# Optimization experiments

Hardware: AMD Instinct MI355X
Metric: run time of the kernel (lower is better)

Reference implementation:

```python
import jax, jax.numpy as jnp
import numpy as np

N_TYPES = 7
DT = 0.1
TAU_INIT = 20.0


def setup_inputs() -> dict:
    key = jax.random.key(0)
    k0, k1, k2, k3 = jax.random.split(key, 4)
    N = 49000          # n_neurons, divisible by 7 types
    E = 1_600_000      # n_edges (~avg degree 32)
    B = 8              # batch (via explicit v_init)
    n_tm1 = N // N_TYPES
    type_ids = (jnp.arange(N) % N_TYPES).astype(jnp.int32)   # type 0 == 'Tm1'
    tm1_indices = jnp.arange(0, N, N_TYPES, dtype=jnp.int32)  # positions where type_ids==0
    return {
        "tm1_input": jax.random.normal(k0, (B, n_tm1), jnp.float32),
        "v_init": jnp.zeros((B, N), jnp.float32),
        "weights": jax.random.normal(k1, (E,), jnp.float32),
        "bias": jnp.zeros((N,), jnp.float32),
        "tau_params": jnp.full((N_TYPES,), TAU_INIT, jnp.float32),
        "scale_excitatory": jnp.ones((), jnp.float32),
        "scale_inhibitory": jnp.ones((), jnp.float32),
        "source_indices": jax.random.randint(k2, (E,), 0, N, dtype=jnp.int32),
        "target_indices": jax.random.randint(k3, (E,), 0, N, dtype=jnp.int32),
        "type_ids": type_ids,
        "tm1_indices": tm1_indices,
        "steps": 100,
    }


def reference(tm1_input, v_init, weights, bias, tau_params,
              scale_excitatory, scale_inhibitory,
              source_indices, target_indices, type_ids, tm1_indices, steps):
    # per-neuron tau from per-type params (torch: get_tau_vector via masks)
    tau = tau_params[type_ids]                                   # [N]
    one = jnp.ones((), weights.dtype)
    edge_scales = jnp.where(weights > 0, scale_excitatory,
                            jnp.where(weights < 0, scale_inhibitory, one))
    scaled_weights = weights * edge_scales                       # [E]

    def step(v, _):
        v = v.at[:, tm1_indices].set(tm1_input)                  # clamp Tm1 neurons
        r = jax.nn.relu(v)                                       # activation
        edge_currents = r[:, source_indices] * scaled_weights    # gather [B,E]
        syn = jnp.zeros_like(v).at[:, target_indices].add(edge_currents)  # scatter-add [B,N]
        dv = (-v + syn + bias) / tau
        dv = dv.at[:, tm1_indices].set(0.0)                      # Tm1 held fixed
        return v + DT * dv, None

    v, _ = jax.lax.scan(step, v_init, None, length=steps)
    return v
```

## Files before the change

kernel.cpp:

```cpp
#include <hip/hip_runtime.h>


#define BLK 256
#define STEPS 100
#define NBATCH 8
#define PRE2 2
static constexpr float DT_C = 0.1f;

__device__ __forceinline__ unsigned f2bf_rne(float x) {
    unsigned u = __float_as_uint(x);
    return (u + 0x7FFFu + ((u >> 16) & 1u)) >> 16;
}
__device__ __forceinline__ unsigned pk_bf2(float a, float b) {
    return f2bf_rne(a) | (f2bf_rne(b) << 16);
}

__global__ void k_zero(int* counts, int* countS, int* tm1_pos, int N) {
    int i = blockIdx.x * BLK + threadIdx.x;
    if (i < N) { counts[i] = 0; countS[i] = 0; tm1_pos[i] = -1; }
}

__global__ void k_tm1pos(const int* __restrict__ tm1_idx, int* tm1_pos, int NT) {
    int i = blockIdx.x * BLK + threadIdx.x;
    if (i < NT) tm1_pos[tm1_idx[i]] = i;
}

__global__ void k_hist(const int* __restrict__ srcI, const int* __restrict__ tgt,
                       const int* __restrict__ type_ids,
                       int* counts, int* countS, unsigned char* __restrict__ flagA,
                       int E) {
    int i = blockIdx.x * BLK + threadIdx.x;
    if (i >= E) return;
    int t = tgt[i];
    atomicAdd(&counts[t], 1);
    unsigned char st = (type_ids[srcI[i]] == 0) ? 1 : 0;
    if (st) atomicAdd(&countS[t], 1);
    flagA[i] = st;
}

__global__ void k_scan1(const int* __restrict__ counts, int* offsets, int* bsum, int N) {
    __shared__ int s[BLK];
    int tx = threadIdx.x;
    int i = blockIdx.x * BLK + tx;
    int v = (i < N) ? counts[i] : 0;
    s[tx] = v; __syncthreads();
    for (int d = 1; d < BLK; d <<= 1) {
        int t = (tx >= d) ? s[tx - d] : 0;
        __syncthreads();
        s[tx] += t;
        __syncthreads();
    }
    if (i < N) offsets[i] = s[tx] - v;
    if (tx == BLK - 1) bsum[blockIdx.x] = s[tx];
}

__global__ void k_scan2(int* bsum, int nb) {
    __shared__ int s[BLK];
    int tx = threadIdx.x;
    int v = (tx < nb) ? bsum[tx] : 0;
    s[tx] = v; __syncthreads();
    for (int d = 1; d < BLK; d <<= 1) {
        int t = (tx >= d) ? s[tx - d] : 0;
        __syncthreads();
        s[tx] += t;
        __syncthreads();
    }
    if (tx < nb) bsum[tx] = s[tx] - v;
}

__global__ void k_scan3(const int* __restrict__ bsum, int* offsets, int N, int E) {
    int i = blockIdx.x * BLK + threadIdx.x;
    if (i < N) {
        offsets[i] += bsum[i >> 8];
    } else if (i == N) {
        offsets[N] = E;
    }
}

__global__ void k_cursors(const int* __restrict__ offsets, const int* __restrict__ countS,
                          int* cursorD, int* cursorS, int* dynEnd, int N) {
    int i = blockIdx.x * BLK + threadIdx.x;
    if (i >= N) return;
    int o  = offsets[i];
    int dE = offsets[i + 1] - countS[i];
    cursorD[i] = o;
    cursorS[i] = dE;
    dynEnd[i]  = dE;
}

__global__ void k_fill(const int* __restrict__ srcI, const int* __restrict__ tgtI,
                       const float* __restrict__ w,
                       const float* __restrict__ se, const float* __restrict__ si,
                       const unsigned char* __restrict__ flagA,
                       int* cursorD, int* cursorS, unsigned* __restrict__ csr, int E) {
    int i = blockIdx.x * BLK + threadIdx.x;
    if (i >= E) return;
    float wv = w[i];
    float sc = wv > 0.f ? se[0] : (wv < 0.f ? si[0] : 1.f);
    float sw = wv * sc;
    unsigned entry = (f2bf_rne(sw) << 16) | (unsigned)srcI[i];
    int t = tgtI[i];
    int pos = flagA[i] ? atomicAdd(&cursorS[t], 1) : atomicAdd(&cursorD[t], 1);
    csr[pos] = entry;
}

__global__ void k_initv(const float* __restrict__ tm1_in, const float* __restrict__ v_init,
                        const float* __restrict__ tau_p,
                        const int* __restrict__ type_ids, const int* __restrict__ tm1_pos,
                        float* __restrict__ v_w, uint4* __restrict__ r0, uint4* __restrict__ r1,
                        float4* __restrict__ coef, int N, int NT) {
    int n = blockIdx.x * BLK + threadIdx.x;
    if (n >= N) return;
    int k = tm1_pos[n];
    float g = DT_C / tau_p[type_ids[n]];
    coef[n] = make_float4(1.f - g, g, (k >= 0) ? 1.f : 0.f, 0.f);
    float vv[NBATCH], rr[NBATCH];
    for (int b = 0; b < NBATCH; ++b) {
        float val = (k >= 0) ? tm1_in[b * NT + k] : v_init[b * N + n];
        vv[b] = val;
        rr[b] = fmaxf(val, 0.f);
    }
    float4* vp = (float4*)(v_w + (size_t)n * 8);
    vp[0] = make_float4(vv[0], vv[1], vv[2], vv[3]);
    vp[1] = make_float4(vv[4], vv[5], vv[6], vv[7]);
    uint4 rq = make_uint4(pk_bf2(rr[0], rr[1]), pk_bf2(rr[2], rr[3]),
                          pk_bf2(rr[4], rr[5]), pk_bf2(rr[6], rr[7]));
    r0[n] = rq;
    r1[n] = rq;
}

__device__ __forceinline__ float butterfly8(float4 a0, float4 a1, int sub) {
    int bit0 = sub & 1, bit1 = (sub >> 1) & 1, bit2 = (sub >> 2) & 1;
    float b0 = (bit0 ? a0.y : a0.x) + __shfl_xor(bit0 ? a0.x : a0.y, 1);
    float b1 = (bit0 ? a0.w : a0.z) + __shfl_xor(bit0 ? a0.z : a0.w, 1);
    float b2 = (bit0 ? a1.y : a1.x) + __shfl_xor(bit0 ? a1.x : a1.y, 1);
    float b3 = (bit0 ? a1.w : a1.z) + __shfl_xor(bit0 ? a1.z : a1.w, 1);
    float c0 = (bit1 ? b1 : b0) + __shfl_xor(bit1 ? b0 : b1, 2);
    float c1 = (bit1 ? b3 : b2) + __shfl_xor(bit1 ? b2 : b3, 2);
    return (bit2 ? c1 : c0) + __shfl_xor(bit2 ? c0 : c1, 4);
}

__global__ void k_static(const int* __restrict__ offsets, const int* __restrict__ dynEnd,
                         const unsigned* __restrict__ csr, const uint4* __restrict__ r0,
                         const float4* __restrict__ coef, const float* __restrict__ bias,
                         float* __restrict__ cF, int N) {
    int tid = blockIdx.x * BLK + threadIdx.x;
    int n = tid >> 3;
    int sub = threadIdx.x & 7;
    if (n >= N) return;
    float4 cf = coef[n];
    int s = dynEnd[n], e = offsets[n + 1];
    float4 a0 = make_float4(0.f, 0.f, 0.f, 0.f);
    float4 a1 = make_float4(0.f, 0.f, 0.f, 0.f);
    for (int i = s + sub; i < e; i += 8) {
        unsigned ew = csr[i];
        float w = __uint_as_float(ew & 0xFFFF0000u);
        uint4 q = r0[ew & 0xFFFFu];
        a0.x = fmaf(w, __uint_as_float(q.x << 16),          a0.x);
        a0.y = fmaf(w, __uint_as_float(q.x & 0xFFFF0000u),  a0.y);
        a0.z = fmaf(w, __uint_as_float(q.y << 16),          a0.z);
        a0.w = fmaf(w, __uint_as_float(q.y & 0xFFFF0000u),  a0.w);
        a1.x = fmaf(w, __uint_as_float(q.z << 16),          a1.x);
        a1.y = fmaf(w, __uint_as_float(q.z & 0xFFFF0000u),  a1.y);
        a1.z = fmaf(w, __uint_as_float(q.w << 16),          a1.z);
        a1.w = fmaf(w, __uint_as_float(q.w & 0xFFFF0000u),  a1.w);
    }
    float syn = butterfly8(a0, a1, sub);
    cF[(size_t)n * 8 + sub] = (syn + bias[n]) * cf.y;
}

__global__ __launch_bounds__(BLK, 8) void k_step(
        const int* __restrict__ offsets, const int* __restrict__ dynEnd,
        const unsigned* __restrict__ csr,
        const float4* __restrict__ coef, const float* __restrict__ cF,
        const uint4* __restrict__ r_prev,
        float* __restrict__ v_w, unsigned short* __restrict__ r_next, int N) {
    int tid = blockIdx.x * BLK + threadIdx.x;
    int n = tid >> 4;
    if (n >= N) return;
    int s16 = threadIdx.x & 15;
    int sub = s16 & 7;
    float4 cf = coef[n];
    if (cf.z != 0.f) return;
    int s = offsets[n], e = dynEnd[n];

    float wj[PRE2];
    int   sj[PRE2];
    #pragma unroll
    for (int j = 0; j < PRE2; ++j) {
        int idx = s + s16 + 16 * j;
        unsigned ew = (idx < e) ? csr[idx] : 0u;
        wj[j] = __uint_as_float(ew & 0xFFFF0000u);
        sj[j] = (int)(ew & 0xFFFFu);
    }
    uint4 q[PRE2];
    #pragma unroll
    for (int j = 0; j < PRE2; ++j) {
        int idx = s + s16 + 16 * j;
        q[j] = (idx < e) ? r_prev[sj[j]] : make_uint4(0u, 0u, 0u, 0u);
    }
    float4 a0 = make_float4(0.f, 0.f, 0.f, 0.f);
    float4 a1 = make_float4(0.f, 0.f, 0.f, 0.f);
    #pragma unroll
    for (int j = 0; j < PRE2; ++j) {
        float w = wj[j];
        a0.x = fmaf(w, __uint_as_float(q[j].x << 16),          a0.x);
        a0.y = fmaf(w, __uint_as_float(q[j].x & 0xFFFF0000u),  a0.y);
        a0.z = fmaf(w, __uint_as_float(q[j].y << 16),          a0.z);
        a0.w = fmaf(w, __uint_as_float(q[j].y & 0xFFFF0000u),  a0.w);
        a1.x = fmaf(w, __uint_as_float(q[j].z << 16),          a1.x);
        a1.y = fmaf(w, __uint_as_float(q[j].z & 0xFFFF0000u),  a1.y);
        a1.z = fmaf(w, __uint_as_float(q[j].w << 16),          a1.z);
        a1.w = fmaf(w, __uint_as_float(q[j].w & 0xFFFF0000u),  a1.w);
    }
    for (int i = s + s16 + 16 * PRE2; i < e; i += 16) {
        unsigned ew = csr[i];
        float w = __uint_as_float(ew & 0xFFFF0000u);
        uint4 qq = r_prev[ew & 0xFFFFu];
        a0.x = fmaf(w, __uint_as_float(qq.x << 16),          a0.x);
        a0.y = fmaf(w, __uint_as_float(qq.x & 0xFFFF0000u),  a0.y);
        a0.z = fmaf(w, __uint_as_float(qq.y << 16),          a0.z);
        a0.w = fmaf(w, __uint_as_float(qq.y & 0xFFFF0000u),  a0.w);
        a1.x = fmaf(w, __uint_as_float(qq.z << 16),          a1.x);
        a1.y = fmaf(w, __uint_as_float(qq.z & 0xFFFF0000u),  a1.y);
        a1.z = fmaf(w, __uint_as_float(qq.w << 16),          a1.z);
        a1.w = fmaf(w, __uint_as_float(qq.w & 0xFFFF0000u),  a1.w);
    }
    float syn = butterfly8(a0, a1, sub);
    syn += __shfl_xor(syn, 8);
    if (s16 < 8) {
        size_t idx = (size_t)n * 8 + sub;
        float vn = v_w[idx] * cf.x + syn * cf.y + cF[idx];
        v_w[idx] = vn;
        r_next[idx] = (unsigned short)f2bf_rne(fmaxf(vn, 0.f));
    }
}

__global__ void k_out(const float* __restrict__ v_w, float* __restrict__ out, int N) {
    int t = blockIdx.x * BLK + threadIdx.x;
    if (t >= NBATCH * N) return;
    int b = t / N;
    int n = t - b * N;
    out[t] = v_w[(size_t)n * 8 + b];
}

static inline size_t align16(size_t x) { return (x + 15) & ~(size_t)15; }

extern "C" void kernel_launch(void* const* d_in, const int* in_sizes, int n_in,
                              void* d_out, int out_size, void* d_ws, size_t ws_size,
                              hipStream_t stream) {
    const float* tm1_in  = (const float*)d_in[0];
    const float* v_init  = (const float*)d_in[1];
    const float* weights = (const float*)d_in[2];
    const float* bias    = (const float*)d_in[3];
    const float* tau_p   = (const float*)d_in[4];
    const float* se      = (const float*)d_in[5];
    const float* si      = (const float*)d_in[6];
    const int*   srcI    = (const int*)d_in[7];
    const int*   tgtI    = (const int*)d_in[8];
    const int*   type_ids= (const int*)d_in[9];
    const int*   tm1_idx = (const int*)d_in[10];

    const int E  = in_sizes[2];
    const int N  = in_sizes[3];
    const int NT = in_sizes[10];

    char* p = (char*)d_ws;
    size_t off = 0;
    auto take = [&](size_t bytes) { void* r = p + off; off += align16(bytes); return r; };
    int*      offsets = (int*)     take((size_t)(N + 1) * 4);
    int*      cursorD = (int*)     take((size_t)N * 4);
    int*      cursorS = (int*)     take((size_t)N * 4);
    int*      counts  = (int*)     take((size_t)N * 4);
    int*      countS  = (int*)     take((size_t)N * 4);
    int*      dynEnd  = (int*)     take((size_t)N * 4);
    int*      tm1_pos = (int*)     take((size_t)N * 4);
    int*      bsum    = (int*)     take(1024 * 4);
    unsigned char* flagA = (unsigned char*)take((size_t)E);
    unsigned* csr     = (unsigned*)take((size_t)E * 4);
    float4*   coef    = (float4*)  take((size_t)N * 16);
    float*    cF      = (float*)   take((size_t)N * 8 * 4);
    float*    v_w     = (float*)   take((size_t)N * 8 * 4);
    uint4*    r0      = (uint4*)   take((size_t)N * 16);
    uint4*    r1      = (uint4*)   take((size_t)N * 16);
    (void)ws_size;

    const int gN  = (N + BLK - 1) / BLK;
    const int gN1 = (N + 1 + BLK - 1) / BLK;
    const int gE  = (E + BLK - 1) / BLK;
    const int gNT = (NT + BLK - 1) / BLK;
    const int g8  = (N * 8 + BLK - 1) / BLK;
    const int g16 = (N * 16 + BLK - 1) / BLK;

    k_zero<<<gN, BLK, 0, stream>>>(counts, countS, tm1_pos, N);
    k_tm1pos<<<gNT, BLK, 0, stream>>>(tm1_idx, tm1_pos, NT);
    k_hist<<<gE, BLK, 0, stream>>>(srcI, tgtI, type_ids, counts, countS, flagA, E);
    k_scan1<<<gN, BLK, 0, stream>>>(counts, offsets, bsum, N);
    k_scan2<<<1, BLK, 0, stream>>>(bsum, gN);
    k_scan3<<<gN1, BLK, 0, stream>>>(bsum, offsets, N, E);
    k_cursors<<<gN, BLK, 0, stream>>>(offsets, countS, cursorD, cursorS, dynEnd, N);
    k_fill<<<gE, BLK, 0, stream>>>(srcI, tgtI, weights, se, si, flagA,
                                   cursorD, cursorS, csr, E);
    k_initv<<<gN, BLK, 0, stream>>>(tm1_in, v_init, tau_p, type_ids, tm1_pos,
                                    v_w, r0, r1, coef, N, NT);
    k_static<<<g8, BLK, 0, stream>>>(offsets, dynEnd, csr, r0, coef, bias, cF, N);

    uint4* rb[2] = { r0, r1 };
    for (int s = 0; s < STEPS; ++s) {
        k_step<<<g16, BLK, 0, stream>>>(offsets, dynEnd, csr, coef, cF, rb[s & 1],
                                        v_w, (unsigned short*)rb[(s + 1) & 1], N);
    }
    k_out<<<g8, BLK, 0, stream>>>(v_w, (float*)d_out, N);
}
```

Baseline: 1.251 ms.

## Stage per-batch activations in LDS and switch to batch-major state layout

The per-step kernel now launches one 1024-thread block per (batch, chunk) pair. Each block copies that batch's full bf16 activation vector (about 98KB) into shared memory and gathers source activations from LDS instead of global uint4 loads. State is moved to batch-major layout and written directly into the output buffer, which removes the final transpose kernel. In exchange, the CSR index and weight stream is read once per batch instead of once for all 8 batches, the grid shrinks to 256 large blocks, and every step pays an LDS fill, which may leave CUs underused.

After: 3.228 ms. 158% more time.

```diff
diff --git a/kernel.cpp b/kernel.cpp
--- a/kernel.cpp
+++ b/kernel.cpp
@@ -2,17 +2,14 @@
 
 
 #define BLK 256
+#define SBLK 1024
 #define STEPS 100
 #define NBATCH 8
-#define PRE2 2
 static constexpr float DT_C = 0.1f;
 
 __device__ __forceinline__ unsigned f2bf_rne(float x) {
     unsigned u = __float_as_uint(x);
     return (u + 0x7FFFu + ((u >> 16) & 1u)) >> 16;
-}
-__device__ __forceinline__ unsigned pk_bf2(float a, float b) {
-    return f2bf_rne(a) | (f2bf_rne(b) << 16);
 }
 
 __global__ void k_zero(int* counts, int* countS, int* tm1_pos, int N) {
@@ -104,29 +101,35 @@
     csr[pos] = entry;
 }
 
-__global__ void k_initv(const float* __restrict__ tm1_in, const float* __restrict__ v_init,
-                        const float* __restrict__ tau_p,
-                        const int* __restrict__ type_ids, const int* __restrict__ tm1_pos,
-                        float* __restrict__ v_w, uint4* __restrict__ r0, uint4* __restrict__ r1,
-                        float4* __restrict__ coef, int N, int NT) {
+__global__ void k_initp(const float* __restrict__ tm1_in, const float* __restrict__ v_init,
+                        const int* __restrict__ tm1_pos,
+                        float* __restrict__ v, unsigned short* __restrict__ r0p,
+                        unsigned short* __restrict__ r1p, int N, int NT) {
     int n = blockIdx.x * BLK + threadIdx.x;
     if (n >= N) return;
+    int b = blockIdx.y;
     int k = tm1_pos[n];
+    float val = (k >= 0) ? tm1_in[(size_t)b * NT + k] : v_init[(size_t)b * N + n];
+    size_t ix = (size_t)b * N + n;
+    v[ix] = val;
+    unsigned short rr = (unsigned short)f2bf_rne(fmaxf(val, 0.f));
+    r0p[ix] = rr;
+    r1p[ix] = rr;
+}
+
+__global__ void k_rows(const unsigned short* __restrict__ r0p,
+                       const int* __restrict__ tm1_pos, const int* __restrict__ type_ids,
+                       const float* __restrict__ tau_p,
+                       uint4* __restrict__ rows, float2* __restrict__ coef2, int N) {
+    int n = blockIdx.x * BLK + threadIdx.x;
+    if (n >= N) return;
+    unsigned rr[8];
+    #pragma unroll
+    for (int b = 0; b < 8; ++b) rr[b] = r0p[(size_t)b * N + n];
+    rows[n] = make_uint4(rr[0] | (rr[1] << 16), rr[2] | (rr[3] << 16),
+                         rr[4] | (rr[5] << 16), rr[6] | (rr[7] << 16));
     float g = DT_C / tau_p[type_ids[n]];
-    coef[n] = make_float4(1.f - g, g, (k >= 0) ? 1.f : 0.f, 0.f);
-    float vv[NBATCH], rr[NBATCH];
-    for (int b = 0; b < NBATCH; ++b) {
-        float val = (k >= 0) ? tm1_in[b * NT + k] : v_init[b * N + n];
-        vv[b] = val;
-        rr[b] = fmaxf(val, 0.f);
-    }
-    float4* vp = (float4*)(v_w + (size_t)n * 8);
-    vp[0] = make_float4(vv[0], vv[1], vv[2], vv[3]);
-    vp[1] = make_float4(vv[4], vv[5], vv[6], vv[7]);
-    uint4 rq = make_uint4(pk_bf2(rr[0], rr[1]), pk_bf2(rr[2], rr[3]),
-                          pk_bf2(rr[4], rr[5]), pk_bf2(rr[6], rr[7]));
-    r0[n] = rq;
-    r1[n] = rq;
+    coef2[n] = make_float2((tm1_pos[n] >= 0) ? 0.f : (1.f - g), g);
 }
 
 __device__ __forceinline__ float butterfly8(float4 a0, float4 a1, int sub) {
@@ -141,21 +144,21 @@
 }
 
 __global__ void k_static(const int* __restrict__ offsets, const int* __restrict__ dynEnd,
-                         const unsigned* __restrict__ csr, const uint4* __restrict__ r0,
-                         const float4* __restrict__ coef, const float* __restrict__ bias,
+                         const unsigned* __restrict__ csr, const uint4* __restrict__ rows,
+                         const float2* __restrict__ coef2, const float* __restrict__ bias,
                          float* __restrict__ cF, int N) {
     int tid = blockIdx.x * BLK + threadIdx.x;
     int n = tid >> 3;
     int sub = threadIdx.x & 7;
     if (n >= N) return;
-    float4 cf = coef[n];
+    float g = coef2[n].y;
     int s = dynEnd[n], e = offsets[n + 1];
     float4 a0 = make_float4(0.f, 0.f, 0.f, 0.f);
     float4 a1 = make_float4(0.f, 0.f, 0.f, 0.f);
     for (int i = s + sub; i < e; i += 8) {
         unsigned ew = csr[i];
         float w = __uint_as_float(ew & 0xFFFF0000u);
-        uint4 q = r0[ew & 0xFFFFu];
+        uint4 q = rows[ew & 0xFFFFu];
         a0.x = fmaf(w, __uint_as_float(q.x << 16),          a0.x);
         a0.y = fmaf(w, __uint_as_float(q.x & 0xFFFF0000u),  a0.y);
         a0.z = fmaf(w, __uint_as_float(q.y << 16),          a0.z);
@@ -166,82 +169,56 @@
         a1.w = fmaf(w, __uint_as_float(q.w & 0xFFFF0000u),  a1.w);
     }
     float syn = butterfly8(a0, a1, sub);
-    cF[(size_t)n * 8 + sub] = (syn + bias[n]) * cf.y;
-}
-
-__global__ __launch_bounds__(BLK, 8) void k_step(
+    cF[(size_t)sub * N + n] = (syn + bias[n]) * g;
+}
+
+__global__ __launch_bounds__(SBLK) void k_step_lds(
         const int* __restrict__ offsets, const int* __restrict__ dynEnd,
         const unsigned* __restrict__ csr,
-        const float4* __restrict__ coef, const float* __restrict__ cF,
-        const uint4* __restrict__ r_prev,
-        float* __restrict__ v_w, unsigned short* __restrict__ r_next, int N) {
-    int tid = blockIdx.x * BLK + threadIdx.x;
-    int n = tid >> 4;
-    if (n >= N) return;
-    int s16 = threadIdx.x & 15;
-    int sub = s16 & 7;
-    float4 cf = coef[n];
-    if (cf.z != 0.f) return;
-    int s = offsets[n], e = dynEnd[n];
-
-    float wj[PRE2];
-    int   sj[PRE2];
-    #pragma unroll
-    for (int j = 0; j < PRE2; ++j) {
-        int idx = s + s16 + 16 * j;
-        unsigned ew = (idx < e) ? csr[idx] : 0u;
-        wj[j] = __uint_as_float(ew & 0xFFFF0000u);
-        sj[j] = (int)(ew & 0xFFFFu);
-    }
-    uint4 q[PRE2];
-    #pragma unroll
-    for (int j = 0; j < PRE2; ++j) {
-        int idx = s + s16 + 16 * j;
-        q[j] = (idx < e) ? r_prev[sj[j]] : make_uint4(0u, 0u, 0u, 0u);
-    }
-    float4 a0 = make_float4(0.f, 0.f, 0.f, 0.f);
-    float4 a1 = make_float4(0.f, 0.f, 0.f, 0.f);
-    #pragma unroll
-    for (int j = 0; j < PRE2; ++j) {
-        float w = wj[j];
-        a0.x = fmaf(w, __uint_as_float(q[j].x << 16),          a0.x);
-        a0.y = fmaf(w, __uint_as_float(q[j].x & 0xFFFF0000u),  a0.y);
-        a0.z = fmaf(w, __uint_as_float(q[j].y << 16),          a0.z);
-        a0.w = fmaf(w, __uint_as_float(q[j].y & 0xFFFF0000u),  a0.w);
-        a1.x = fmaf(w, __uint_as_float(q[j].z << 16),          a1.x);
-        a1.y = fmaf(w, __uint_as_float(q[j].z & 0xFFFF0000u),  a1.y);
-        a1.z = fmaf(w, __uint_as_float(q[j].w << 16),          a1.z);
-        a1.w = fmaf(w, __uint_as_float(q[j].w & 0xFFFF0000u),  a1.w);
-    }
-    for (int i = s + s16 + 16 * PRE2; i < e; i += 16) {
-        unsigned ew = csr[i];
-        float w = __uint_as_float(ew & 0xFFFF0000u);
-        uint4 qq = r_prev[ew & 0xFFFFu];
-        a0.x = fmaf(w, __uint_as_float(qq.x << 16),          a0.x);
-        a0.y = fmaf(w, __uint_as_float(qq.x & 0xFFFF0000u),  a0.y);
-        a0.z = fmaf(w, __uint_as_float(qq.y << 16),          a0.z);
-        a0.w = fmaf(w, __uint_as_float(qq.y & 0xFFFF0000u),  a0.w);
-        a1.x = fmaf(w, __uint_as_float(qq.z << 16),          a1.x);
-        a1.y = fmaf(w, __uint_as_float(qq.z & 0xFFFF0000u),  a1.y);
-        a1.z = fmaf(w, __uint_as_float(qq.w << 16),          a1.z);
-        a1.w = fmaf(w, __uint_as_float(qq.w & 0xFFFF0000u),  a1.w);
-    }
-    float syn = butterfly8(a0, a1, sub);
-    syn += __shfl_xor(syn, 8);
-    if (s16 < 8) {
-        size_t idx = (size_t)n * 8 + sub;
-        float vn = v_w[idx] * cf.x + syn * cf.y + cF[idx];
-        v_w[idx] = vn;
-        r_next[idx] = (unsigned short)f2bf_rne(fmaxf(vn, 0.f));
-    }
-}
-
-__global__ void k_out(const float* __restrict__ v_w, float* __restrict__ out, int N) {
-    int t = blockIdx.x * BLK + threadIdx.x;
-    if (t >= NBATCH * N) return;
-    int b = t / N;
-    int n = t - b * N;
-    out[t] = v_w[(size_t)n * 8 + b];
+        const float2* __restrict__ coef2, const float* __restrict__ cF,
+        const unsigned short* __restrict__ r_prev,
+        float* __restrict__ v, unsigned short* __restrict__ r_next,
+        int N, int M, int CH) {
+    extern __shared__ unsigned short lr[];
+    int blk = blockIdx.x;
+    int b = blk >> 5;
+    int c = blk & 31;
+    const unsigned short* rp = r_prev + (size_t)b * N;
+    const uint4* s4 = (const uint4*)rp;
+    uint4* d4 = (uint4*)lr;
+    int n4 = M >> 3;
+    for (int i = threadIdx.x; i < n4; i += SBLK) d4[i] = s4[i];
+    __syncthreads();
+
+    int n0 = c * CH;
+    int nEnd = n0 + CH; if (nEnd > N) nEnd = N;
+    int g  = threadIdx.x >> 4;
+    int sl = threadIdx.x & 15;
+    for (int n = n0 + g; n < nEnd; n += SBLK / 16) {
+        float2 cf = coef2[n];
+        if (cf.x == 0.f) continue;
+        int s = offsets[n], e = dynEnd[n];
+        float acc = 0.f;
+        for (int idx = s + sl; idx < e; idx += 16) {
+            unsigned ew = csr[idx];
+            int srcn = (int)(ew & 0xFFFFu);
+            float w = __uint_as_float(ew & 0xFFFF0000u);
+            float rv;
+            if (srcn < M) rv = __uint_as_float((unsigned)lr[srcn] << 16);
+            else          rv = __uint_as_float((unsigned)rp[srcn] << 16);
+            acc = fmaf(w, rv, acc);
+        }
+        acc += __shfl_xor(acc, 1);
+        acc += __shfl_xor(acc, 2);
+        acc += __shfl_xor(acc, 4);
+        acc += __shfl_xor(acc, 8);
+        if (sl == 0) {
+            size_t ix = (size_t)b * N + n;
+            float vn = v[ix] * cf.x + acc * cf.y + cF[ix];
+            v[ix] = vn;
+            r_next[ix] = (unsigned short)f2bf_rne(fmaxf(vn, 0.f));
+        }
+    }
 }
 
 static inline size_t align16(size_t x) { return (x + 15) & ~(size_t)15; }
@@ -278,19 +255,20 @@
     int*      bsum    = (int*)     take(1024 * 4);
     unsigned char* flagA = (unsigned char*)take((size_t)E);
     unsigned* csr     = (unsigned*)take((size_t)E * 4);
-    float4*   coef    = (float4*)  take((size_t)N * 16);
+    float2*   coef2   = (float2*)  take((size_t)N * 8);
+    uint4*    rows    = (uint4*)   take((size_t)N * 16);
     float*    cF      = (float*)   take((size_t)N * 8 * 4);
-    float*    v_w     = (float*)   take((size_t)N * 8 * 4);
-    uint4*    r0      = (uint4*)   take((size_t)N * 16);
-    uint4*    r1      = (uint4*)   take((size_t)N * 16);
+    unsigned short* r0p = (unsigned short*)take((size_t)N * 8 * 2);
+    unsigned short* r1p = (unsigned short*)take((size_t)N * 8 * 2);
     (void)ws_size;
+
+    float* v = (float*)d_out;
 
     const int gN  = (N + BLK - 1) / BLK;
     const int gN1 = (N + 1 + BLK - 1) / BLK;
     const int gE  = (E + BLK - 1) / BLK;
     const int gNT = (NT + BLK - 1) / BLK;
     const int g8  = (N * 8 + BLK - 1) / BLK;
-    const int g16 = (N * 16 + BLK - 1) / BLK;
 
     k_zero<<<gN, BLK, 0, stream>>>(counts, countS, tm1_pos, N);
     k_tm1pos<<<gNT, BLK, 0, stream>>>(tm1_idx, tm1_pos, NT);
@@ -301,14 +279,31 @@
     k_cursors<<<gN, BLK, 0, stream>>>(offsets, countS, cursorD, cursorS, dynEnd, N);
     k_fill<<<gE, BLK, 0, stream>>>(srcI, tgtI, weights, se, si, flagA,
                                    cursorD, cursorS, csr, E);
-    k_initv<<<gN, BLK, 0, stream>>>(tm1_in, v_init, tau_p, type_ids, tm1_pos,
-                                    v_w, r0, r1, coef, N, NT);
-    k_static<<<g8, BLK, 0, stream>>>(offsets, dynEnd, csr, r0, coef, bias, cF, N);
-
-    uint4* rb[2] = { r0, r1 };
+    k_initp<<<dim3(gN, NBATCH), BLK, 0, stream>>>(tm1_in, v_init, tm1_pos,
+                                                  v, r0p, r1p, N, NT);
+    k_rows<<<gN, BLK, 0, stream>>>(r0p, tm1_pos, type_ids, tau_p, rows, coef2, N);
+    k_static<<<g8, BLK, 0, stream>>>(offsets, dynEnd, csr, rows, coef2, bias, cF, N);
+
+    int dev = 0, maxShm = 0;
+    hipGetDevice(&dev);
+    hipDeviceGetAttribute(&maxShm, hipDeviceAttributeMaxSharedMemoryPerBlock, dev);
+    size_t want = (size_t)N * 2;
+    int cap = maxShm;
+    if ((size_t)cap < want) {
+        if (hipFuncSetAttribute((const void*)k_step_lds,
+                                hipFuncAttributeMaxDynamicSharedMemorySize,
+                                (int)want) == hipSuccess)
+            cap = (int)want;
+    }
+    int M = N;
+    if ((size_t)cap < want) M = (cap / 2) & ~7;
+    size_t shm = (size_t)M * 2;
+
+    const int CH = (N + 31) / 32;
+    unsigned short* rb[2] = { r0p, r1p };
     for (int s = 0; s < STEPS; ++s) {
-        k_step<<<g16, BLK, 0, stream>>>(offsets, dynEnd, csr, coef, cF, rb[s & 1],
-                                        v_w, (unsigned short*)rb[(s + 1) & 1], N);
-    }
-    k_out<<<g8, BLK, 0, stream>>>(v_w, (float*)d_out, N);
-}
+        k_step_lds<<<NBATCH * 32, SBLK, shm, stream>>>(
+            offsets, dynEnd, csr, coef2, cF, rb[s & 1], v, rb[(s + 1) & 1],
+            N, M, CH);
+    }
+}
```

## Use 8 lanes per neuron in step kernel with deeper prefetch and nontemporal loads

Applied to the files above, without the earlier changes.

The per-step kernel now assigns 8 threads per neuron instead of 16, which halves the grid and removes the extra cross-half shuffle and the idle half-wavefront in the epilogue. Edge prefetch depth rises from 2 to 5 per lane. CSR, v and cF accesses use nontemporal loads and stores. The per-neuron coefficient shrinks from float4 to float2, with the Tm1 flag encoded as a zero decay factor. Fewer lanes per neuron lengthens each lane's serial gather chain, which trades parallelism for per-lane memory-level parallelism. The launch-bounds occupancy hint was also dropped.

After: 1.234 ms. No clear change (-1.3%).

```diff
diff --git a/kernel.cpp b/kernel.cpp
--- a/kernel.cpp
+++ b/kernel.cpp
@@ -4,8 +4,10 @@
 #define BLK 256
 #define STEPS 100
 #define NBATCH 8
-#define PRE2 2
+#define PRE 5
 static constexpr float DT_C = 0.1f;
+
+typedef unsigned uv4 __attribute__((ext_vector_type(4)));
 
 __device__ __forceinline__ unsigned f2bf_rne(float x) {
     unsigned u = __float_as_uint(x);
@@ -68,13 +70,14 @@
     if (tx < nb) bsum[tx] = s[tx] - v;
 }
 
-__global__ void k_scan3(const int* __restrict__ bsum, int* offsets, int N, int E) {
-    int i = blockIdx.x * BLK + threadIdx.x;
-    if (i < N) {
-        offsets[i] += bsum[i >> 8];
-    } else if (i == N) {
-        offsets[N] = E;
-    }
+__global__ void k_scan3c(const int* __restrict__ bsum, const int* __restrict__ countS,
+                         int* offsets, int* cursorD, int* cursorS, int* dynEnd,
+                         int N, int E) {
+    int i = blockIdx.x * BLK + threadIdx.x;
+    if (i > N) return;
+    if (i == N) { offsets[N] = E; return; }
+    int o = offsets[i] + bsum[i >> 8];
+    offsets[i] = o;
 }
 
 __global__ void k_cursors(const int* __restrict__ offsets, const int* __restrict__ countS,
@@ -108,12 +111,12 @@
                         const float* __restrict__ tau_p,
                         const int* __restrict__ type_ids, const int* __restrict__ tm1_pos,
                         float* __restrict__ v_w, uint4* __restrict__ r0, uint4* __restrict__ r1,
-                        float4* __restrict__ coef, int N, int NT) {
+                        float2* __restrict__ coef2, int N, int NT) {
     int n = blockIdx.x * BLK + threadIdx.x;
     if (n >= N) return;
     int k = tm1_pos[n];
     float g = DT_C / tau_p[type_ids[n]];
-    coef[n] = make_float4(1.f - g, g, (k >= 0) ? 1.f : 0.f, 0.f);
+    coef2[n] = make_float2((k >= 0) ? 0.f : (1.f - g), g);
     float vv[NBATCH], rr[NBATCH];
     for (int b = 0; b < NBATCH; ++b) {
         float val = (k >= 0) ? tm1_in[b * NT + k] : v_init[b * N + n];
@@ -142,13 +145,13 @@
 
 __global__ void k_static(const int* __restrict__ offsets, const int* __restrict__ dynEnd,
                          const unsigned* __restrict__ csr, const uint4* __restrict__ r0,
-                         const float4* __restrict__ coef, const float* __restrict__ bias,
+                         const float2* __restrict__ coef2, const float* __restrict__ bias,
                          float* __restrict__ cF, int N) {
     int tid = blockIdx.x * BLK + threadIdx.x;
     int n = tid >> 3;
     int sub = threadIdx.x & 7;
     if (n >= N) return;
-    float4 cf = coef[n];
+    float g = coef2[n].y;
     int s = dynEnd[n], e = offsets[n + 1];
     float4 a0 = make_float4(0.f, 0.f, 0.f, 0.f);
     float4 a1 = make_float4(0.f, 0.f, 0.f, 0.f);
@@ -166,43 +169,42 @@
         a1.w = fmaf(w, __uint_as_float(q.w & 0xFFFF0000u),  a1.w);
     }
     float syn = butterfly8(a0, a1, sub);
-    cF[(size_t)n * 8 + sub] = (syn + bias[n]) * cf.y;
-}
-
-__global__ __launch_bounds__(BLK, 8) void k_step(
+    cF[(size_t)n * 8 + sub] = (syn + bias[n]) * g;
+}
+
+__global__ __launch_bounds__(BLK) void k_step(
         const int* __restrict__ offsets, const int* __restrict__ dynEnd,
         const unsigned* __restrict__ csr,
-        const float4* __restrict__ coef, const float* __restrict__ cF,
-        const uint4* __restrict__ r_prev,
+        const float2* __restrict__ coef2, const float* __restrict__ cF,
+        const uv4* __restrict__ r_prev,
         float* __restrict__ v_w, unsigned short* __restrict__ r_next, int N) {
     int tid = blockIdx.x * BLK + threadIdx.x;
-    int n = tid >> 4;
+    int n = tid >> 3;
+    int sub = threadIdx.x & 7;
     if (n >= N) return;
-    int s16 = threadIdx.x & 15;
-    int sub = s16 & 7;
-    float4 cf = coef[n];
-    if (cf.z != 0.f) return;
+    float2 cf = coef2[n];
+    if (cf.x == 0.f) return;
     int s = offsets[n], e = dynEnd[n];
 
-    float wj[PRE2];
-    int   sj[PRE2];
+    float wj[PRE];
+    int   sj[PRE];
     #pragma unroll
-    for (int j = 0; j < PRE2; ++j) {
-        int idx = s + s16 + 16 * j;
-        unsigned ew = (idx < e) ? csr[idx] : 0u;
+    for (int j = 0; j < PRE; ++j) {
+        int idx = s + sub + 8 * j;
+        unsigned ew = (idx < e) ? __builtin_nontemporal_load(csr + idx) : 0u;
         wj[j] = __uint_as_float(ew & 0xFFFF0000u);
         sj[j] = (int)(ew & 0xFFFFu);
     }
-    uint4 q[PRE2];
+    uv4 q[PRE];
     #pragma unroll
-    for (int j = 0; j < PRE2; ++j) {
-        int idx = s + s16 + 16 * j;
-        q[j] = (idx < e) ? r_prev[sj[j]] : make_uint4(0u, 0u, 0u, 0u);
+    for (int j = 0; j < PRE; ++j) {
+        int idx = s + sub + 8 * j;
+        q[j] = (idx < e) ? r_prev[sj[j]] : (uv4)(0u);
     }
     float4 a0 = make_float4(0.f, 0.f, 0.f, 0.f);
     float4 a1 = make_float4(0.f, 0.f, 0.f, 0.f);
     #pragma unroll
-    for (int j = 0; j < PRE2; ++j) {
+    for (int j = 0; j < PRE; ++j) {
         float w = wj[j];
         a0.x = fmaf(w, __uint_as_float(q[j].x << 16),          a0.x);
         a0.y = fmaf(w, __uint_as_float(q[j].x & 0xFFFF0000u),  a0.y);
@@ -213,10 +215,10 @@
         a1.z = fmaf(w, __uint_as_float(q[j].w << 16),          a1.z);
         a1.w = fmaf(w, __uint_as_float(q[j].w & 0xFFFF0000u),  a1.w);
     }
-    for (int i = s + s16 + 16 * PRE2; i < e; i += 16) {
-        unsigned ew = csr[i];
+    for (int i = s + sub + 8 * PRE; i < e; i += 8) {
+        unsigned ew = __builtin_nontemporal_load(csr + i);
         float w = __uint_as_float(ew & 0xFFFF0000u);
-        uint4 qq = r_prev[ew & 0xFFFFu];
+        uv4 qq = r_prev[ew & 0xFFFFu];
         a0.x = fmaf(w, __uint_as_float(qq.x << 16),          a0.x);
         a0.y = fmaf(w, __uint_as_float(qq.x & 0xFFFF0000u),  a0.y);
         a0.z = fmaf(w, __uint_as_float(qq.y << 16),          a0.z);
@@ -227,13 +229,12 @@
         a1.w = fmaf(w, __uint_as_float(qq.w & 0xFFFF0000u),  a1.w);
     }
     float syn = butterfly8(a0, a1, sub);
-    syn += __shfl_xor(syn, 8);
-    if (s16 < 8) {
-        size_t idx = (size_t)n * 8 + sub;
-        float vn = v_w[idx] * cf.x + syn * cf.y + cF[idx];
-        v_w[idx] = vn;
-        r_next[idx] = (unsigned short)f2bf_rne(fmaxf(vn, 0.f));
-    }
+    size_t idx = (size_t)n * 8 + sub;
+    float vo = __builtin_nontemporal_load(v_w + idx);
+    float cf3 = __builtin_nontemporal_load(cF + idx);
+    float vn = vo * cf.x + syn * cf.y + cf3;
+    __builtin_nontemporal_store(vn, v_w + idx);
+    r_next[idx] = (unsigned short)f2bf_rne(fmaxf(vn, 0.f));
 }
 
 __global__ void k_out(const float* __restrict__ v_w, float* __restrict__ out, int N) {
@@ -278,7 +279,7 @@
     int*      bsum    = (int*)     take(1024 * 4);
     unsigned char* flagA = (unsigned char*)take((size_t)E);
     unsigned* csr     = (unsigned*)take((size_t)E * 4);
-    float4*   coef    = (float4*)  take((size_t)N * 16);
+    float2*   coef2   = (float2*)  take((size_t)N * 8);
     float*    cF      = (float*)   take((size_t)N * 8 * 4);
     float*    v_w     = (float*)   take((size_t)N * 8 * 4);
     uint4*    r0      = (uint4*)   take((size_t)N * 16);
@@ -290,25 +291,26 @@
     const int gE  = (E + BLK - 1) / BLK;
     const int gNT = (NT + BLK - 1) / BLK;
     const int g8  = (N * 8 + BLK - 1) / BLK;
-    const int g16 = (N * 16 + BLK - 1) / BLK;
 
     k_zero<<<gN, BLK, 0, stream>>>(counts, countS, tm1_pos, N);
     k_tm1pos<<<gNT, BLK, 0, stream>>>(tm1_idx, tm1_pos, NT);
     k_hist<<<gE, BLK, 0, stream>>>(srcI, tgtI, type_ids, counts, countS, flagA, E);
     k_scan1<<<gN, BLK, 0, stream>>>(counts, offsets, bsum, N);
     k_scan2<<<1, BLK, 0, stream>>>(bsum, gN);
-    k_scan3<<<gN1, BLK, 0, stream>>>(bsum, offsets, N, E);
+    k_scan3c<<<gN1, BLK, 0, stream>>>(bsum, countS, offsets, cursorD, cursorS,
+                                      dynEnd, N, E);
     k_cursors<<<gN, BLK, 0, stream>>>(offsets, countS, cursorD, cursorS, dynEnd, N);
     k_fill<<<gE, BLK, 0, stream>>>(srcI, tgtI, weights, se, si, flagA,
                                    cursorD, cursorS, csr, E);
     k_initv<<<gN, BLK, 0, stream>>>(tm1_in, v_init, tau_p, type_ids, tm1_pos,
-                                    v_w, r0, r1, coef, N, NT);
-    k_static<<<g8, BLK, 0, stream>>>(offsets, dynEnd, csr, r0, coef, bias, cF, N);
+                                    v_w, r0, r1, coef2, N, NT);
+    k_static<<<g8, BLK, 0, stream>>>(offsets, dynEnd, csr, r0, coef2, bias, cF, N);
 
     uint4* rb[2] = { r0, r1 };
     for (int s = 0; s < STEPS; ++s) {
-        k_step<<<g16, BLK, 0, stream>>>(offsets, dynEnd, csr, coef, cF, rb[s & 1],
-                                        v_w, (unsigned short*)rb[(s + 1) & 1], N);
+        k_step<<<g8, BLK, 0, stream>>>(offsets, dynEnd, csr, coef2, cF,
+                                       (const uv4*)rb[s & 1], v_w,
+                                       (unsigned short*)rb[(s + 1) & 1], N);
     }
     k_out<<<g8, BLK, 0, stream>>>(v_w, (float*)d_out, N);
 }
```
